# Optimization experiments

Hardware: AMD Instinct MI355X
Metric: run time of the kernel (lower is better)

The kernel has to match this reference:

```python
import jax, jax.numpy as jnp
import numpy as np

N, C, HW = 32, 256, 64          # batch, in_channels, input_size
K = 128                          # n_clusters
S = 8                            # blocks per side
BLOCK = (HW + S - 1) // S        # = 8, padding_size = 0


def setup_inputs() -> dict:
    key = jax.random.key(0)
    k1, k2 = jax.random.split(key)
    x = jax.random.normal(k1, (N, C, HW, HW), dtype=jnp.float32)
    cluster_centers = jax.random.normal(k2, (K, C), dtype=jnp.float32)
    return {"x": x, "cluster_centers": cluster_centers}


def reference(x, cluster_centers):
    # --- Codebook: argmin over squared distances, computed without the
    x2 = jnp.sum(x * x, axis=1)                       # (N, H, W)
    c2 = jnp.sum(cluster_centers * cluster_centers, axis=1)  # (K,)
    xc = jnp.einsum('nchw,kc->nkhw', x, cluster_centers)     # (N, K, H, W)
    dist = x2[:, None] - 2.0 * xc + c2[None, :, None, None]
    code = jnp.argmin(dist, axis=1)                   # (N, H, W) int

    # --- BlockWiseHistogramEncoder: unfold into S*S non-overlapping
    # BLOCKxBLOCK blocks (padding_size == 0 here), one_hot(code+1), mean ---
    shifted = code + 1                                # values in [1, K]
    n = shifted.shape[0]
    blocks = shifted.reshape(n, S, BLOCK, S, BLOCK)
    blocks = blocks.transpose(0, 1, 3, 2, 4).reshape(n, S * S, BLOCK * BLOCK)
    onehot = (blocks[..., None] == jnp.arange(K + 1)).astype(jnp.float32)
    return onehot.mean(axis=2)                        # (N, S*S, K+1)
```

## Files before the change

### kernel.cpp

```cpp
#include <hip/hip_runtime.h>

#define C_DIM 256
#define K_DIM 128
#define HW_DIM 64
#define PIX 4096
#define N_IMG 32
#define ROWU 36

using short8 = __attribute__((ext_vector_type(8))) short;
using f32x4  = __attribute__((ext_vector_type(4))) float;

union frag_u { unsigned long long u[2]; short8 s; };

__device__ __forceinline__ unsigned rne_bf16(float v) {
    unsigned u = __float_as_uint(v);
    return (u + 0x7fffu + ((u >> 16) & 1u)) >> 16;
}
__device__ __forceinline__ float bf_up(unsigned h) { return __uint_as_float(h << 16); }

__device__ __forceinline__ void split3(float v, unsigned& h, unsigned& m, unsigned& l) {
    h = rne_bf16(v);
    float r1 = v - bf_up(h);
    m = rne_bf16(r1);
    float r2 = r1 - bf_up(m);
    l = rne_bf16(r2);
}

__device__ __forceinline__ unsigned long long umin64(unsigned long long a, unsigned long long b) {
    return a < b ? a : b;
}
__device__ __forceinline__ unsigned mono(float d) {
    unsigned u = __float_as_uint(d);
    return u ^ ((u & 0x80000000u) ? 0xFFFFFFFFu : 0x80000000u);
}

__global__ __launch_bounds__(64) void prep_kernel(const float* __restrict__ cl,
                                                  unsigned short* __restrict__ Bt,
                                                  float* __restrict__ c2) {
    int k = blockIdx.x;
    int lane = threadIdx.x;
    const float4* row = (const float4*)(cl + k * C_DIM);
    float4 v = row[lane];
    float vv[4] = {v.x, v.y, v.z, v.w};
    unsigned short* bk = Bt + k * 768 + lane * 4;
#pragma unroll
    for (int i = 0; i < 4; ++i) {
        unsigned h, m, l;
        split3(vv[i], h, m, l);
        bk[i]       = (unsigned short)h;
        bk[256 + i] = (unsigned short)m;
        bk[512 + i] = (unsigned short)l;
    }
    if (lane == 0) {
        float s = 0.f;
#pragma unroll
        for (int i = 0; i < C_DIM / 4; ++i) {
            float4 u = row[i];
            s = fmaf(u.x, u.x, s);
            s = fmaf(u.y, u.y, s);
            s = fmaf(u.z, u.z, s);
            s = fmaf(u.w, u.w, s);
        }
        c2[k] = s;
    }
}

__global__ __launch_bounds__(256) void main_kernel(
    const float* __restrict__ x, const unsigned short* __restrict__ Bt,
    const float* __restrict__ c2v, unsigned char* __restrict__ code) {

    __shared__ unsigned short Ap[2][3][128 * ROWU];
    __shared__ float x2p[2][128];
    __shared__ unsigned long long red[4][128];

    const int t    = threadIdx.x;
    const int lane = t & 63;
    const int w    = t >> 6;
    const int q    = lane >> 4;
    const int l15  = lane & 15;

    const int px = t & 127;
    const int h  = t >> 7;

    const int b   = blockIdx.x;
    const int img = b >> 5;
    const int pb  = (b & 31) * 128;

    const float* xg = x + (size_t)img * (C_DIM * PIX) + pb + px;

    f32x4 acc[8][2];
#pragma unroll
    for (int m = 0; m < 8; ++m)
#pragma unroll
        for (int ns = 0; ns < 2; ++ns) acc[m][ns] = (f32x4){0.f, 0.f, 0.f, 0.f};

    float xr[16];
#pragma unroll
    for (int j = 0; j < 16; ++j) xr[j] = xg[(size_t)(h * 16 + j) * PIX];

    float x2part = 0.f;
    const unsigned short* bt0 = Bt + (w * 32 + l15) * 768 + q * 8;
    const unsigned short* bt1 = bt0 + 16 * 768;

#pragma unroll 2
    for (int ci = 0; ci < 8; ++ci) {
        const int par = ci & 1;

#pragma unroll
        for (int g = 0; g < 2; ++g) {
            unsigned pk0[4], pk1[4], pk2[4];
#pragma unroll
            for (int jj = 0; jj < 4; ++jj) {
                float v0 = xr[g * 8 + jj * 2], v1 = xr[g * 8 + jj * 2 + 1];
                unsigned h0, m0, l0, h1, m1, l1;
                split3(v0, h0, m0, l0);
                split3(v1, h1, m1, l1);
                pk0[jj] = h0 | (h1 << 16);
                pk1[jj] = m0 | (m1 << 16);
                pk2[jj] = l0 | (l1 << 16);
                x2part = fmaf(v0, v0, x2part);
                x2part = fmaf(v1, v1, x2part);
            }
            int base = px * ROWU + h * 16 + g * 8;
            *(uint2*)&Ap[par][0][base]     = make_uint2(pk0[0], pk0[1]);
            *(uint2*)&Ap[par][0][base + 4] = make_uint2(pk0[2], pk0[3]);
            *(uint2*)&Ap[par][1][base]     = make_uint2(pk1[0], pk1[1]);
            *(uint2*)&Ap[par][1][base + 4] = make_uint2(pk1[2], pk1[3]);
            *(uint2*)&Ap[par][2][base]     = make_uint2(pk2[0], pk2[1]);
            *(uint2*)&Ap[par][2][base + 4] = make_uint2(pk2[2], pk2[3]);
        }
        if (ci == 7) x2p[h][px] = x2part;

        float xr2[16];
        if (ci < 7) {
#pragma unroll
            for (int j = 0; j < 16; ++j)
                xr2[j] = xg[(size_t)((ci + 1) * 32 + h * 16 + j) * PIX];
        }

        __syncthreads();

#pragma unroll
        for (int pa = 0; pa < 3; ++pa) {
            const int npb = (pa == 0) ? 3 : ((pa == 1) ? 2 : 1);
            frag_u bf[3][2];
#pragma unroll
            for (int pbp = 0; pbp < 3; ++pbp) {
                if (pbp < npb) {
                    const int ko = pbp * 256 + ci * 32;
                    bf[pbp][0].s = *(const short8*)(bt0 + ko);
                    bf[pbp][1].s = *(const short8*)(bt1 + ko);
                }
            }
#pragma unroll
            for (int m = 0; m < 8; ++m) {
                const unsigned short* ap = &Ap[par][pa][(m * 16 + l15) * ROWU + q * 8];
                frag_u af;
                af.u[0] = *(const unsigned long long*)ap;
                af.u[1] = *(const unsigned long long*)(ap + 4);
#pragma unroll
                for (int pbp = 0; pbp < 3; ++pbp) {
                    if (pbp < npb) {
                        acc[m][0] = __builtin_amdgcn_mfma_f32_16x16x32_bf16(af.s, bf[pbp][0].s, acc[m][0], 0, 0, 0);
                        acc[m][1] = __builtin_amdgcn_mfma_f32_16x16x32_bf16(af.s, bf[pbp][1].s, acc[m][1], 0, 0, 0);
                    }
                }
            }
        }
        if (ci < 7) {
#pragma unroll
            for (int j = 0; j < 16; ++j) xr[j] = xr2[j];
        }
    }

    __syncthreads();

    const float c2a0 = c2v[w * 32 + l15];
    const float c2a1 = c2v[w * 32 + 16 + l15];
    const unsigned n0 = (unsigned)(w * 32 + l15);
    const unsigned n1 = n0 + 16;

#pragma unroll
    for (int m = 0; m < 8; ++m) {
#pragma unroll
        for (int r = 0; r < 4; ++r) {
            int pxl = m * 16 + q * 4 + r;
            float x2v = x2p[0][pxl] + x2p[1][pxl];
            float d0 = (x2v - 2.0f * acc[m][0][r]) + c2a0;
            float d1 = (x2v - 2.0f * acc[m][1][r]) + c2a1;
            unsigned long long k0 = ((unsigned long long)mono(d0) << 32) | n0;
            unsigned long long k1 = ((unsigned long long)mono(d1) << 32) | n1;
            unsigned long long best = umin64(k0, k1);
            best = umin64(best, __shfl_xor(best, 1));
            best = umin64(best, __shfl_xor(best, 2));
            best = umin64(best, __shfl_xor(best, 4));
            best = umin64(best, __shfl_xor(best, 8));
            if (l15 == 0) red[w][pxl] = best;
        }
    }
    __syncthreads();

    if (t < 128) {
        unsigned long long m0 = umin64(umin64(red[0][t], red[1][t]),
                                       umin64(red[2][t], red[3][t]));
        code[(size_t)img * PIX + pb + t] = (unsigned char)(m0 & 0xFFu);
    }
}

__global__ __launch_bounds__(256) void hist_kernel(const unsigned char* __restrict__ code,
                                                   float* __restrict__ out) {
    __shared__ int hist[4][K_DIM + 1];
    int wid = threadIdx.x >> 6, lane = threadIdx.x & 63;
    int b = blockIdx.x * 4 + wid;
    int n = b >> 6, sy = (b >> 3) & 7, sx = b & 7;

    hist[wid][lane] = 0;
    hist[wid][lane + 64] = 0;
    if (lane == 0) hist[wid][128] = 0;
    __syncthreads();

    int hh = sy * 8 + (lane >> 3);
    int ww = sx * 8 + (lane & 7);
    int c = code[n * PIX + hh * HW_DIM + ww];
    atomicAdd(&hist[wid][c + 1], 1);
    __syncthreads();

    const float inv = 1.0f / 64.0f;
    out[(size_t)b * (K_DIM + 1) + lane] = hist[wid][lane] * inv;
    out[(size_t)b * (K_DIM + 1) + 64 + lane] = hist[wid][lane + 64] * inv;
    if (lane == 0) out[(size_t)b * (K_DIM + 1) + 128] = hist[wid][128] * inv;
}

extern "C" void kernel_launch(void* const* d_in, const int* in_sizes, int n_in,
                              void* d_out, int out_size, void* d_ws, size_t ws_size,
                              hipStream_t stream) {
    const float* x  = (const float*)d_in[0];
    const float* cl = (const float*)d_in[1];
    float* out = (float*)d_out;

    unsigned short* Bt = (unsigned short*)d_ws;
    float* c2 = (float*)((char*)d_ws + 196608);
    unsigned char* code = (unsigned char*)d_ws + 197120;

    prep_kernel<<<K_DIM, 64, 0, stream>>>(cl, Bt, c2);
    main_kernel<<<(N_IMG * PIX) / 128, 256, 0, stream>>>(x, Bt, c2, code);
    hist_kernel<<<(N_IMG * 64) / 4, 256, 0, stream>>>(code, out);
}
```

Before: 228.5 us.

## Single-buffer LDS A tiles with 16B rows and hoist B fragment loads

Drops the double-buffered A tile in shared memory in favour of a single buffer with a barrier at the end of each chunk, and pads rows to 40 elements so A fragments can be written and read as 16-byte vectors. B fragments for all three precision planes are loaded once at the top of each chunk iteration instead of inside the MFMA loop, and the chunk loop is no longer unrolled. This halves LDS usage, which may allow more resident blocks, and reduces the LDS instruction count. The cost is an extra barrier per iteration and less overlap between the split/store phase and the MFMA phase.

```diff
diff --git a/kernel.cpp b/kernel.cpp
--- a/kernel.cpp
+++ b/kernel.cpp
@@ -5,12 +5,10 @@
 #define HW_DIM 64
 #define PIX 4096
 #define N_IMG 32
-#define ROWU 36
+#define ROWU 40
 
 using short8 = __attribute__((ext_vector_type(8))) short;
 using f32x4  = __attribute__((ext_vector_type(4))) float;
-
-union frag_u { unsigned long long u[2]; short8 s; };
 
 __device__ __forceinline__ unsigned rne_bf16(float v) {
     unsigned u = __float_as_uint(v);
@@ -69,7 +67,7 @@
     const float* __restrict__ x, const unsigned short* __restrict__ Bt,
     const float* __restrict__ c2v, unsigned char* __restrict__ code) {
 
-    __shared__ unsigned short Ap[2][3][128 * ROWU];
+    __shared__ __align__(16) unsigned short Ap[3][128 * ROWU];
     __shared__ float x2p[2][128];
     __shared__ unsigned long long red[4][128];
 
@@ -99,12 +97,17 @@
     for (int j = 0; j < 16; ++j) xr[j] = xg[(size_t)(h * 16 + j) * PIX];
 
     float x2part = 0.f;
-    const unsigned short* bt0 = Bt + (w * 32 + l15) * 768 + q * 8;
-    const unsigned short* bt1 = bt0 + 16 * 768;
-
-#pragma unroll 2
+    const unsigned short* btb = Bt + (w * 32 + l15) * 768 + q * 8;
+
+    short8 bv[3][2];
+
+#pragma unroll 1
     for (int ci = 0; ci < 8; ++ci) {
-        const int par = ci & 1;
+#pragma unroll
+        for (int p = 0; p < 3; ++p) {
+            bv[p][0] = *(const short8*)(btb + p * 256 + ci * 32);
+            bv[p][1] = *(const short8*)(btb + 16 * 768 + p * 256 + ci * 32);
+        }
 
 #pragma unroll
         for (int g = 0; g < 2; ++g) {
@@ -122,20 +125,16 @@
                 x2part = fmaf(v1, v1, x2part);
             }
             int base = px * ROWU + h * 16 + g * 8;
-            *(uint2*)&Ap[par][0][base]     = make_uint2(pk0[0], pk0[1]);
-            *(uint2*)&Ap[par][0][base + 4] = make_uint2(pk0[2], pk0[3]);
-            *(uint2*)&Ap[par][1][base]     = make_uint2(pk1[0], pk1[1]);
-            *(uint2*)&Ap[par][1][base + 4] = make_uint2(pk1[2], pk1[3]);
-            *(uint2*)&Ap[par][2][base]     = make_uint2(pk2[0], pk2[1]);
-            *(uint2*)&Ap[par][2][base + 4] = make_uint2(pk2[2], pk2[3]);
+            *(uint4*)&Ap[0][base] = make_uint4(pk0[0], pk0[1], pk0[2], pk0[3]);
+            *(uint4*)&Ap[1][base] = make_uint4(pk1[0], pk1[1], pk1[2], pk1[3]);
+            *(uint4*)&Ap[2][base] = make_uint4(pk2[0], pk2[1], pk2[2], pk2[3]);
         }
         if (ci == 7) x2p[h][px] = x2part;
 
-        float xr2[16];
         if (ci < 7) {
 #pragma unroll
             for (int j = 0; j < 16; ++j)
-                xr2[j] = xg[(size_t)((ci + 1) * 32 + h * 16 + j) * PIX];
+                xr[j] = xg[(size_t)((ci + 1) * 32 + h * 16 + j) * PIX];
         }
 
         __syncthreads();
@@ -143,37 +142,20 @@
 #pragma unroll
         for (int pa = 0; pa < 3; ++pa) {
             const int npb = (pa == 0) ? 3 : ((pa == 1) ? 2 : 1);
-            frag_u bf[3][2];
-#pragma unroll
-            for (int pbp = 0; pbp < 3; ++pbp) {
-                if (pbp < npb) {
-                    const int ko = pbp * 256 + ci * 32;
-                    bf[pbp][0].s = *(const short8*)(bt0 + ko);
-                    bf[pbp][1].s = *(const short8*)(bt1 + ko);
-                }
-            }
 #pragma unroll
             for (int m = 0; m < 8; ++m) {
-                const unsigned short* ap = &Ap[par][pa][(m * 16 + l15) * ROWU + q * 8];
-                frag_u af;
-                af.u[0] = *(const unsigned long long*)ap;
-                af.u[1] = *(const unsigned long long*)(ap + 4);
-#pragma unroll
-                for (int pbp = 0; pbp < 3; ++pbp) {
-                    if (pbp < npb) {
-                        acc[m][0] = __builtin_amdgcn_mfma_f32_16x16x32_bf16(af.s, bf[pbp][0].s, acc[m][0], 0, 0, 0);
-                        acc[m][1] = __builtin_amdgcn_mfma_f32_16x16x32_bf16(af.s, bf[pbp][1].s, acc[m][1], 0, 0, 0);
+                short8 af = *(const short8*)&Ap[pa][(m * 16 + l15) * ROWU + q * 8];
+#pragma unroll
+                for (int pb2 = 0; pb2 < 3; ++pb2) {
+                    if (pb2 < npb) {
+                        acc[m][0] = __builtin_amdgcn_mfma_f32_16x16x32_bf16(af, bv[pb2][0], acc[m][0], 0, 0, 0);
+                        acc[m][1] = __builtin_amdgcn_mfma_f32_16x16x32_bf16(af, bv[pb2][1], acc[m][1], 0, 0, 0);
                     }
                 }
             }
         }
-        if (ci < 7) {
-#pragma unroll
-            for (int j = 0; j < 16; ++j) xr[j] = xr2[j];
-        }
-    }
-
-    __syncthreads();
+        __syncthreads();
+    }
 
     const float c2a0 = c2v[w * 32 + l15];
     const float c2a1 = c2v[w * 32 + 16 + l15];
```

Result: no change. 228.2 us (-0.2%).
